# Optimization experiments

Measured on AMD Instinct MI355X. Metric: run time of the kernel, lower is better.

## Reference

```python
import jax, jax.numpy as jnp
import numpy as np

B, T, C, H = 16, 512, 256, 8
HS_T = C // H   # temporal head size = 32
HS_S = T // H   # spatial head size = 64
EPS = 1e-6


def _ln(x, w, b):
    m = x.mean(-1, keepdims=True)
    v = ((x - m) ** 2).mean(-1, keepdims=True)
    return (x - m) / jnp.sqrt(v + EPS) * w + b


def setup_inputs() -> dict:
    key = jax.random.key(0)
    ks = jax.random.split(key, 16)
    rn = lambda k, s, scale: jax.random.normal(k, s, dtype=jnp.float32) * scale
    inp = {
        "x_T": rn(ks[0], (B, T, C), 1.0),
        "x_S": rn(ks[1], (B, C, T), 1.0),
        # temporal attention: per-head q/k/v projections, stacked [H, hs, C]
        "Wq_t": rn(ks[2], (H, HS_T, C), C ** -0.5),
        "Wk_t": rn(ks[3], (H, HS_T, C), C ** -0.5),
        "Wv_t": rn(ks[4], (H, HS_T, C), C ** -0.5),
        "Wo": rn(ks[5], (C, C), C ** -0.5),
        # spatial attention: per-head q/k over the time axis, stacked [H, hs_s, T]
        "Wq_s": rn(ks[6], (H, HS_S, T), T ** -0.5),
        "Wk_s": rn(ks[7], (H, HS_S, T), T ** -0.5),
        # feed-forward blocks (expansion_factor=4)
        "ff1_w1": rn(ks[8], (4 * C, C), C ** -0.5),
        "ff1_b1": jnp.zeros((4 * C,), jnp.float32),
        "ff1_w2": rn(ks[9], (C, 4 * C), (4 * C) ** -0.5),
        "ff1_b2": jnp.zeros((C,), jnp.float32),
        "ff2_w1": rn(ks[10], (4 * C, C), C ** -0.5),
        "ff2_b1": jnp.zeros((4 * C,), jnp.float32),
        "ff2_w2": rn(ks[11], (C, 4 * C), (4 * C) ** -0.5),
        "ff2_b2": jnp.zeros((C,), jnp.float32),
        # layernorm affine params
        "t_ln1_w": jnp.ones((C,), jnp.float32), "t_ln1_b": jnp.zeros((C,), jnp.float32),
        "t_ln2_w": jnp.ones((C,), jnp.float32), "t_ln2_b": jnp.zeros((C,), jnp.float32),
        "s_ln1_w": jnp.ones((T,), jnp.float32), "s_ln1_b": jnp.zeros((T,), jnp.float32),
        "fus_ln_w": jnp.ones((C,), jnp.float32), "fus_ln_b": jnp.zeros((C,), jnp.float32),
    }
    return inp


def reference(x_T, x_S, Wq_t, Wk_t, Wv_t, Wo, Wq_s, Wk_s,
              ff1_w1, ff1_b1, ff1_w2, ff1_b2, ff2_w1, ff2_b1, ff2_w2, ff2_b2,
              t_ln1_w, t_ln1_b, t_ln2_w, t_ln2_b, s_ln1_w, s_ln1_b,
              fus_ln_w, fus_ln_b):
    # ---- temporal (causal) multi-head attention ----
    h = _ln(x_T, t_ln1_w, t_ln1_b)                         # [B,T,C]
    q = jnp.einsum('btc,hdc->bhtd', h, Wq_t)
    k = jnp.einsum('btc,hdc->bhtd', h, Wk_t)
    v = jnp.einsum('btc,hdc->bhtd', h, Wv_t)
    scores = jnp.einsum('bhtd,bhsd->bhts', q, k) / jnp.sqrt(jnp.float32(HS_T))
    causal = jnp.tril(jnp.ones((T, T), dtype=bool))
    scores = jnp.where(causal, scores, -jnp.inf)
    att = jax.nn.softmax(scores, axis=-1)
    o = jnp.einsum('bhts,bhsd->bhtd', att, v)              # [B,H,T,hs]
    o = o.transpose(0, 2, 1, 3).reshape(B, T, C)           # concat heads
    attn_out = o @ Wo.T
    x = x_T + attn_out
    # FFN 1
    h2 = _ln(x, t_ln2_w, t_ln2_b)
    f = jax.nn.relu(h2 @ ff1_w1.T + ff1_b1) @ ff1_w2.T + ff1_b2
    temporal_out = x + f                                   # [B,T,C]
    # ---- spatial (non-causal) attention over neurons ----
    hs = _ln(x_S, s_ln1_w, s_ln1_b)                        # [B,C,T]
    qs = jnp.einsum('bct,hdt->bhcd', hs, Wq_s)
    ks = jnp.einsum('bct,hdt->bhcd', hs, Wk_s)
    sc = jnp.einsum('bhcd,bhed->bhce', qs, ks) / jnp.sqrt(jnp.float32(HS_S))
    spatial_weights = jax.nn.softmax(sc, axis=-1).mean(axis=1)   # [B,C,C], mean over heads
    # ---- fusion ----
    fused = jnp.einsum('bce,bte->btc', spatial_weights, temporal_out)
    x2 = temporal_out + fused
    h3 = _ln(x2, fus_ln_w, fus_ln_b)
    f2 = jax.nn.relu(h3 @ ff2_w1.T + ff2_b1) @ ff2_w2.T + ff2_b2
    out = x2 + f2
    return out, spatial_weights
```

## Files before the change

kernel.cpp:

```cpp
#include <hip/hip_runtime.h>
#include <hip/hip_bf16.h>

typedef __hip_bfloat16 bf16;
typedef __attribute__((ext_vector_type(8))) short short8;
typedef __attribute__((ext_vector_type(4))) float f32x4;

#define F_BIAS 1
#define F_RELU 2
#define F_RES  4

__device__ __forceinline__ void st_out(float* p, float v){ *p = v; }
__device__ __forceinline__ void st_out(bf16* p, float v){ *p = __float2bfloat16(v); }
__device__ __forceinline__ short f2bs(float f){
  bf16 h = __float2bfloat16(f);
  return *reinterpret_cast<short*>(&h);
}

__device__ __forceinline__ void gl_lds16(const void* g, void* l){
  __builtin_amdgcn_global_load_lds(
      (const __attribute__((address_space(1))) void*)g,
      (__attribute__((address_space(3))) void*)l, 16, 0, 0);
}

__device__ __forceinline__ void lgkm_barrier(){
  asm volatile("s_waitcnt lgkmcnt(0)" ::: "memory");
  __builtin_amdgcn_s_barrier();
}

struct ProArgs {
  const float* wsrc[10];
  bf16* wdst[10];
  const float *xT, *xS, *tl1w, *tl1b, *sl1w, *sl1b;
  bf16 *hT, *hS;
};

template<int RL>
__device__ __forceinline__ void wave_ln(bf16* __restrict__ dst,
    const float* __restrict__ src, const float* __restrict__ w,
    const float* __restrict__ bvec, int row){
  int lane = threadIdx.x & 63;
  const float* s = src + (size_t)row*RL;
  float4 v0 = *(const float4*)(s + lane*4);
  float4 v1 = {0.f,0.f,0.f,0.f};
  float sum = v0.x+v0.y+v0.z+v0.w;
  float sq  = v0.x*v0.x+v0.y*v0.y+v0.z*v0.z+v0.w*v0.w;
  if (RL == 512){
    v1 = *(const float4*)(s + 256 + lane*4);
    sum += v1.x+v1.y+v1.z+v1.w;
    sq  += v1.x*v1.x+v1.y*v1.y+v1.z*v1.z+v1.w*v1.w;
  }
  #pragma unroll
  for (int off=32; off; off>>=1){
    sum += __shfl_xor(sum, off, 64);
    sq  += __shfl_xor(sq , off, 64);
  }
  const float inv = 1.0f/(float)RL;
  float mean = sum*inv;
  float rstd = rsqrtf(sq*inv - mean*mean + 1e-6f);
  float4 w0 = *(const float4*)(w + lane*4);
  float4 b0 = *(const float4*)(bvec + lane*4);
  bf16* d = dst + (size_t)row*RL;
  short4 o;
  o.x = f2bs((v0.x-mean)*rstd*w0.x + b0.x);
  o.y = f2bs((v0.y-mean)*rstd*w0.y + b0.y);
  o.z = f2bs((v0.z-mean)*rstd*w0.z + b0.z);
  o.w = f2bs((v0.w-mean)*rstd*w0.w + b0.w);
  *(short4*)((short*)d + lane*4) = o;
  if (RL == 512){
    float4 w1 = *(const float4*)(w + 256 + lane*4);
    float4 b1 = *(const float4*)(bvec + 256 + lane*4);
    short4 o1;
    o1.x = f2bs((v1.x-mean)*rstd*w1.x + b1.x);
    o1.y = f2bs((v1.y-mean)*rstd*w1.y + b1.y);
    o1.z = f2bs((v1.z-mean)*rstd*w1.z + b1.z);
    o1.w = f2bs((v1.w-mean)*rstd*w1.w + b1.w);
    *(short4*)((short*)d + 256 + lane*4) = o1;
  }
}

__global__ __launch_bounds__(256) void prologue(ProArgs a){
  int blk = blockIdx.x;
  int wid = threadIdx.x >> 6;
  if (blk < 1792){
    int v = blk*256 + threadIdx.x;
    int e = v*4;
    int seg = (e>=65536)+(e>=131072)+(e>=196608)+(e>=262144)+(e>=524288)
            + (e>=786432)+(e>=1048576)+(e>=1310720)+(e>=1572864);
    const int starts[10] = {0,65536,131072,196608,262144,524288,786432,
                            1048576,1310720,1572864};
    int off = e - starts[seg];
    float4 f = *(const float4*)(a.wsrc[seg] + off);
    short4 o;
    o.x = f2bs(f.x); o.y = f2bs(f.y); o.z = f2bs(f.z); o.w = f2bs(f.w);
    *(short4*)((short*)a.wdst[seg] + off) = o;
  } else if (blk < 1792 + 2048){
    wave_ln<256>(a.hT, a.xT, a.tl1w, a.tl1b, (blk-1792)*4 + wid);
  } else {
    wave_ln<512>(a.hS, a.xS, a.sl1w, a.sl1b, (blk-3840)*4 + wid);
  }
}

template<int BM, int BN, int BK>
__device__ __forceinline__ void gemm_body(
    short* __restrict__ AsB, short* __restrict__ BsB,
    const bf16* __restrict__ A, const bf16* __restrict__ B,
    float* __restrict__ outF, bf16* __restrict__ outB,
    const float* __restrict__ bias, const float* __restrict__ resid,
    int K, int lda, int ldb, int ldc, int flags, int m0, int n0){
  int tid = threadIdx.x;
  int w = tid>>6, lane = tid&63, quad = lane>>4, l16 = lane&15;
  constexpr int MF  = BM/32;
  constexpr int NF  = BN/32;
  constexpr int CPR = BK/8;
  constexpr int CA  = BM*CPR/256;
  constexpr int CB  = BN*CPR/256;
  int wm = (w>>1)*(BM/2), wn = (w&1)*(BN/2);
  f32x4 acc[MF][NF];
  #pragma unroll
  for (int r=0;r<MF;r++)
    #pragma unroll
    for (int j=0;j<NF;j++)
      acc[r][j] = (f32x4){0.f,0.f,0.f,0.f};

  auto stage = [&](int k0, int half){
    short* as = AsB + half*(BM*BK);
    short* bs = BsB + half*(BN*BK);
    #pragma unroll
    for (int c=0;c<CA;c++){
      int ch = tid + c*256;
      int row = ch / CPR, p = ch % CPR;
      gl_lds16(A + (size_t)(m0+row)*lda + k0 + ((p ^ (row&(CPR-1)))*8),
               &as[row*BK + p*8]);
    }
    #pragma unroll
    for (int c=0;c<CB;c++){
      int ch = tid + c*256;
      int row = ch / CPR, p = ch % CPR;
      gl_lds16(B + (size_t)(n0+row)*ldb + k0 + ((p ^ (row&(CPR-1)))*8),
               &bs[row*BK + p*8]);
    }
  };

  stage(0, 0);
  int nk = K / BK;
  for (int t = 0; t < nk; ++t){
    __syncthreads();
    if (t+1 < nk) stage((t+1)*BK, (t+1)&1);
    const short* as = AsB + (t&1)*(BM*BK);
    const short* bs = BsB + (t&1)*(BN*BK);
    #pragma unroll
    for (int ks=0; ks<BK/32; ++ks){
      short8 af[MF], bfr[NF];
      #pragma unroll
      for (int r=0;r<MF;r++){
        int rr = wm + r*16 + l16;
        af[r] = *(short8*)&as[rr*BK + (((ks*4+quad) ^ (rr&(CPR-1)))*8)];
      }
      #pragma unroll
      for (int j=0;j<NF;j++){
        int rr = wn + j*16 + l16;
        bfr[j] = *(short8*)&bs[rr*BK + (((ks*4+quad) ^ (rr&(CPR-1)))*8)];
      }
      #pragma unroll
      for (int r=0;r<MF;r++)
        #pragma unroll
        for (int j=0;j<NF;j++)
          acc[r][j] = __builtin_amdgcn_mfma_f32_16x16x32_bf16(af[r], bfr[j], acc[r][j], 0,0,0);
    }
  }
  #pragma unroll
  for (int r=0;r<MF;r++){
    int mb = m0 + wm + r*16 + quad*4;
    #pragma unroll
    for (int j=0;j<NF;j++){
      int n = n0 + wn + j*16 + l16;
      float bv = (flags & F_BIAS) ? bias[n] : 0.0f;
      #pragma unroll
      for (int e=0;e<4;e++){
        float v = acc[r][j][e] + bv;
        if (flags & F_RELU) v = fmaxf(v, 0.0f);
        long long idx = (long long)(mb+e)*ldc + n;
        if (flags & F_RES) v += resid[idx];
        if (outF) outF[idx] = v;
        if (outB) st_out(outB + idx, v);
      }
    }
  }
}

struct GArgs {
  const bf16 *A, *B;
  float* outF; bf16* outB;
  const float *bias, *resid;
  int K, lda, ldb, ldc, flags, ty;
};
__global__ __launch_bounds__(256) void gemm_dual(GArgs g0, GArgs g1, int n0){
  __shared__ __align__(16) short As[2*128*64];
  __shared__ __align__(16) short Bs[2*128*64];
  int id = blockIdx.x;
  bool first = id < n0;
  const GArgs& g = first ? g0 : g1;
  int t = first ? id : id - n0;
  int bx = t / g.ty, by = t - bx*g.ty;
  gemm_body<128,128,64>(As, Bs, g.A, g.B, g.outF, g.outB, g.bias, g.resid,
                        g.K, g.lda, g.ldb, g.ldc, g.flags, bx*128, by*128);
}

struct LnFfnArgs {
  const bf16 *A;
  const bf16 *Bm;
  const float *resid0;
  const float *lnw, *lnb;
  const bf16 *W1; const float *B1;
  const bf16 *W2; const float *B2;
  float *outF; bf16 *outB;
  long long sA, sB, sR, sO;
};

__global__ __launch_bounds__(512) void lnffn(LnFfnArgs a){
  __shared__ __align__(16) short arena[73728];
  __shared__ float redS[4][32], redQ[4][32];
  int bz = blockIdx.z;
  const bf16* A  = a.A  + (size_t)bz*a.sA;
  const bf16* Bm = a.Bm + (size_t)bz*a.sB;
  long long rbase = (long long)bz*a.sR;
  long long obase = (long long)bz*a.sO;
  int tid = threadIdx.x;
  int w = tid>>6, lane = tid&63, quad = lane>>4, l16 = lane&15;
  int m0 = blockIdx.x*32;
  int wm = (w>>2)*16;
  int wn = (w&3)*64;

  short* As  = arena;
  short* Bs  = arena + 4096;
  short* Hin = arena;
  short* Hs  = arena + 8192;
  short* Bst = arena + 40960;

  f32x4 acc[4];
  #pragma unroll
  for (int j=0;j<4;j++) acc[j] = (f32x4){0.f,0.f,0.f,0.f};

  auto stage0 = [&](int k0, int half){
    short* as = As + half*(32*64);
    short* bs = Bs + half*(256*64);
    if (tid < 256){
      int row = tid >> 3, p = tid & 7;
      gl_lds16(A + (size_t)(m0+row)*256 + k0 + ((p ^ (row&7))*8),
               &as[row*64 + p*8]);
    }
    #pragma unroll
    for (int c=0;c<4;c++){
      int ch = tid + c*512;
      int row = ch >> 3, p = ch & 7;
      gl_lds16(Bm + (size_t)row*256 + k0 + ((p ^ (row&7))*8),
               &bs[row*64 + p*8]);
    }
  };

  stage0(0, 0);
  for (int t = 0; t < 4; ++t){
    __syncthreads();
    if (t+1 < 4) stage0((t+1)*64, (t+1)&1);
    const short* as = As + (t&1)*(32*64);
    const short* bs = Bs + (t&1)*(256*64);
    #pragma unroll
    for (int ks=0; ks<2; ++ks){
      int rr = wm + l16;
      short8 af = *(short8*)&as[rr*64 + (((ks*4+quad) ^ (rr&7))*8)];
      #pragma unroll
      for (int j=0;j<4;j++){
        int rb = wn + j*16 + l16;
        short8 bfr = *(short8*)&bs[rb*64 + (((ks*4+quad) ^ (rb&7))*8)];
        acc[j] = __builtin_amdgcn_mfma_f32_16x16x32_bf16(af, bfr, acc[j], 0,0,0);
      }
    }
  }
  #pragma unroll
  for (int e=0;e<4;e++){
    int row = wm + quad*4 + e;
    float s = 0.f, q2 = 0.f;
    #pragma unroll
    for (int j=0;j<4;j++){
      float v = acc[j][e] + a.resid0[rbase + (long long)(m0+row)*256 + wn + j*16 + l16];
      acc[j][e] = v;
      s += v; q2 += v*v;
    }
    #pragma unroll
    for (int off=1; off<16; off<<=1){
      s  += __shfl_xor(s , off, 16);
      q2 += __shfl_xor(q2, off, 16);
    }
    if (l16==0){ redS[w&3][row] = s; redQ[w&3][row] = q2; }
  }
  __syncthreads();
  #pragma unroll
  for (int e=0;e<4;e++){
    int row = wm + quad*4 + e;
    float tot = redS[0][row] + redS[1][row] + redS[2][row] + redS[3][row];
    float tq  = redQ[0][row] + redQ[1][row] + redQ[2][row] + redQ[3][row];
    float mean = tot * (1.0f/256.0f);
    float var  = tq * (1.0f/256.0f) - mean*mean;
    float rstd = rsqrtf(var + 1e-6f);
    #pragma unroll
    for (int j=0;j<4;j++){
      int col = wn + j*16 + l16;
      float h = (acc[j][e]-mean)*rstd*a.lnw[col] + a.lnb[col];
      int g = col >> 3;
      Hin[row*256 + ((g ^ row)*8) + (col&7)] = f2bs(h);
    }
  }

  auto stageA = [&](int i, int half){
    short* bs = Bst + half*16384;
    int nc = i>>2, kt = i&3;
    #pragma unroll
    for (int c=0;c<2;c++){
      int ch = tid + c*512;
      int row = ch>>3, p = ch&7;
      gl_lds16(a.W1 + (size_t)(nc*128+row)*256 + kt*64 + ((p ^ (row&7))*8),
               &bs[ch*8]);
    }
  };
  stageA(0, 0);
  f32x4 a2[2];
  for (int i=0; i<32; ++i){
    __syncthreads();
    if (i+1 < 32) stageA(i+1, (i+1)&1);
    const short* bs = Bst + (i&1)*16384;
    int kt = i&3, nc = i>>2;
    if (kt==0){
      a2[0] = (f32x4){0.f,0.f,0.f,0.f};
      a2[1] = (f32x4){0.f,0.f,0.f,0.f};
    }
    #pragma unroll
    for (int ks=0; ks<2; ++ks){
      int rr = wm + l16;
      int kk = kt*8 + ks*4 + quad;
      short8 af = *(short8*)&Hin[rr*256 + ((kk ^ rr)*8)];
      #pragma unroll
      for (int j=0;j<2;j++){
        int rb = (w&3)*32 + j*16 + l16;
        short8 bk = *(short8*)&bs[rb*64 + (((ks*4+quad) ^ (rb&7))*8)];
        a2[j] = __builtin_amdgcn_mfma_f32_16x16x32_bf16(af, bk, a2[j], 0,0,0);
      }
    }
    if (kt==3){
      #pragma unroll
      for (int j=0;j<2;j++)
        #pragma unroll
        for (int e=0;e<4;e++){
          int row = wm + quad*4 + e;
          int col = nc*128 + (w&3)*32 + j*16 + l16;
          float v = fmaxf(a2[j][e] + a.B1[col], 0.0f);
          int g = col>>3;
          Hs[row*1024 + ((g ^ (row&7))*8) + (col&7)] = f2bs(v);
        }
    }
  }

  auto stageB = [&](int kt, int half){
    short* bs = Bst + half*16384;
    #pragma unroll
    for (int c=0;c<4;c++){
      int ch = tid + c*512;
      int row = ch>>3, p = ch&7;
      gl_lds16(a.W2 + (size_t)row*1024 + kt*64 + ((p ^ (row&7))*8),
               &bs[ch*8]);
    }
  };
  stageB(0, 0);
  f32x4 accB[4];
  #pragma unroll
  for (int j=0;j<4;j++) accB[j] = (f32x4){0.f,0.f,0.f,0.f};
  for (int kt=0; kt<16; ++kt){
    __syncthreads();
    if (kt+1 < 16) stageB(kt+1, (kt+1)&1);
    const short* bs = Bst + (kt&1)*16384;
    #pragma unroll
    for (int ks=0; ks<2; ++ks){
      int rr = wm + l16;
      int kk = kt*8 + ks*4 + quad;
      short8 af = *(short8*)&Hs[rr*1024 + ((kk ^ (rr&7))*8)];
      #pragma unroll
      for (int j=0;j<4;j++){
        int rb = wn + j*16 + l16;
        short8 bk = *(short8*)&bs[rb*64 + (((ks*4+quad) ^ (rb&7))*8)];
        accB[j] = __builtin_amdgcn_mfma_f32_16x16x32_bf16(af, bk, accB[j], 0,0,0);
      }
    }
  }
  #pragma unroll
  for (int j=0;j<4;j++){
    int n = wn + j*16 + l16;
    float bv = a.B2[n];
    #pragma unroll
    for (int e=0;e<4;e++){
      int row = wm + quad*4 + e;
      long long idx = obase + (long long)(m0+row)*256 + n;
      float v = accB[j][e] + bv + acc[j][e];
      a.outF[idx] = v;
      if (a.outB) st_out(a.outB + idx, v);
    }
  }
}

__device__ __forceinline__ int fsw(int row){ return (row>>1)&3; }
__global__ __launch_bounds__(256) void flash_mfma(
    const bf16* __restrict__ qkv, bf16* __restrict__ o){
  int qt = (int)gridDim.x - 1 - (int)blockIdx.x;
  int h = blockIdx.y, b = blockIdx.z;
  int tid = threadIdx.x;
  int w = tid>>6, lane = tid&63, quad = lane>>4, l16 = lane&15;
  __shared__ __align__(16) bf16 Qs[64*32];
  __shared__ __align__(16) bf16 Ks[2][64*32];
  __shared__ __align__(16) bf16 Vt[2][32*72];
  __shared__ __align__(16) bf16 Ps[64*72];
  const bf16* base = qkv + (size_t)b*512*768;
  int t0 = qt*64;
  int srow = tid>>2, spos = tid&3;
  gl_lds16(base + (size_t)(t0+srow)*768 + h*32 + ((spos ^ fsw(srow))*8),
           &Qs[srow*32 + spos*8]);
  {
    const bf16* rp = base + (size_t)srow*768 + h*32;
    gl_lds16(rp + 256 + ((spos ^ fsw(srow))*8), &Ks[0][srow*32 + spos*8]);
    short8 v = *(const short8*)(rp + 512 + spos*8);
    #pragma unroll
    for (int q=0;q<8;q++){
      short tmp = v[q];
      Vt[0][(spos*8+q)*72 + srow] = *(bf16*)&tmp;
    }
  }
  f32x4 accO[2];
  accO[0] = (f32x4){0.f,0.f,0.f,0.f};
  accO[1] = (f32x4){0.f,0.f,0.f,0.f};
  float m_i[4], l_i[4];
  #pragma unroll
  for (int e=0;e<4;e++){ m_i[e] = -3.0e38f; l_i[e] = 0.0f; }
  const float scale = 0.17677669529663687f;
  __syncthreads();
  int rq = w*16 + l16;
  short8 aq = *(short8*)&Qs[rq*32 + ((quad ^ fsw(rq))*8)];

  for (int kt = 0; kt <= qt; ++kt){
    if (kt) __syncthreads();
    int cur = kt&1, nxt = cur^1;
    bool pre = (kt < qt);
    short8 vpre;
    if (pre){
      const bf16* rp = base + (size_t)((kt+1)*64 + srow)*768 + h*32;
      gl_lds16(rp + 256 + ((spos ^ fsw(srow))*8), &Ks[nxt][srow*32 + spos*8]);
      vpre = *(const short8*)(rp + 512 + spos*8);
    }
    f32x4 S[4];
    #pragma unroll
    for (int j2=0;j2<4;j2++){
      int rk = j2*16 + l16;
      short8 bk = *(short8*)&Ks[cur][rk*32 + ((quad ^ fsw(rk))*8)];
      S[j2] = __builtin_amdgcn_mfma_f32_16x16x32_bf16(aq, bk,
                (f32x4){0.f,0.f,0.f,0.f}, 0,0,0);
    }
    bool diag = (kt == qt);
    int s0 = kt*64;
    int qrow_base = t0 + w*16 + quad*4;
    #pragma unroll
    for (int e=0;e<4;e++){
      float sv[4];
      #pragma unroll
      for (int j2=0;j2<4;j2++){
        float x = S[j2][e]*scale;
        if (diag && (s0 + j2*16 + l16 > qrow_base + e)) x = -3.0e38f;
        sv[j2] = x;
      }
      float mx = fmaxf(fmaxf(sv[0],sv[1]), fmaxf(sv[2],sv[3]));
      #pragma unroll
      for (int off=1; off<16; off<<=1) mx = fmaxf(mx, __shfl_xor(mx, off, 64));
      float m_new = fmaxf(m_i[e], mx);
      float alpha = __expf(m_i[e]-m_new);
      float rs = 0.0f;
      #pragma unroll
      for (int j2=0;j2<4;j2++){
        float p = __expf(sv[j2]-m_new);
        rs += p;
        Ps[(w*16+quad*4+e)*72 + j2*16 + l16] = __float2bfloat16(p);
      }
      #pragma unroll
      for (int off=1; off<16; off<<=1) rs += __shfl_xor(rs, off, 64);
      l_i[e] = l_i[e]*alpha + rs;
      m_i[e] = m_new;
      accO[0][e] *= alpha;
      accO[1][e] *= alpha;
    }
    asm volatile("s_waitcnt lgkmcnt(0)" ::: "memory");
    __builtin_amdgcn_sched_barrier(0);
    #pragma unroll
    for (int sh=0; sh<2; ++sh){
      short8 ap = *(short8*)&Ps[(w*16+l16)*72 + sh*32 + quad*8];
      #pragma unroll
      for (int dh=0; dh<2; ++dh){
        short8 bv = *(short8*)&Vt[cur][(dh*16+l16)*72 + sh*32 + quad*8];
        accO[dh] = __builtin_amdgcn_mfma_f32_16x16x32_bf16(ap, bv, accO[dh], 0,0,0);
      }
    }
    if (pre){
      #pragma unroll
      for (int q=0;q<8;q++){
        short tmp = vpre[q];
        Vt[nxt][(spos*8+q)*72 + srow] = *(bf16*)&tmp;
      }
    }
  }
  #pragma unroll
  for (int e=0;e<4;e++){
    float inv = 1.0f/l_i[e];
    int t = t0 + w*16 + quad*4 + e;
    bf16* op = o + ((size_t)(b*512+t))*256 + h*32 + l16;
    op[0]  = __float2bfloat16(accO[0][e]*inv);
    op[16] = __float2bfloat16(accO[1][e]*inv);
  }
}

__global__ __launch_bounds__(256) void spatial_fused(
    const bf16* __restrict__ qk, float* __restrict__ out1,
    bf16* __restrict__ swB){
  int ct = blockIdx.x & 15, b = blockIdx.x >> 4;
  int tid = threadIdx.x;
  int w = tid>>6, lane = tid&63, quad = lane>>4, l16 = lane&15;
  __shared__ __align__(16) bf16 Qall[16*512];
  __shared__ __align__(16) bf16 Ks[2][256*64];
  __shared__ float redM[4][16], redS2[4][16];
  const bf16* qbase = qk + ((size_t)(b*256 + ct*16))*1024;
  #pragma unroll
  for (int c=0;c<4;c++){
    int ch = tid + c*256;
    int row = ch>>6, p = ch&63;
    gl_lds16(qbase + (size_t)row*1024 + ((p ^ (row&7))*8), &Qall[row*512 + p*8]);
  }
  auto stageK = [&](int h, int half){
    bf16* ks = Ks[half];
    #pragma unroll
    for (int c=0;c<8;c++){
      int ch = tid + c*256;
      int e = ch>>3, p = ch&7;
      gl_lds16(qk + ((size_t)(b*256 + e))*1024 + 512 + h*64 + ((p ^ (e&7))*8),
               &ks[e*64 + p*8]);
    }
  };
  stageK(0, 0);
  float fRes[4][4];
  #pragma unroll
  for (int j=0;j<4;j++)
    #pragma unroll
    for (int e=0;e<4;e++) fRes[j][e] = 0.0f;

  for (int h=0; h<8; ++h){
    __syncthreads();
    if (h+1 < 8) stageK(h+1, (h+1)&1);
    const bf16* kcur = Ks[h&1];
    f32x4 acc[4];
    #pragma unroll
    for (int j=0;j<4;j++) acc[j] = (f32x4){0.f,0.f,0.f,0.f};
    #pragma unroll
    for (int ki=0; ki<2; ++ki){
      int g = h*8 + ki*4 + quad;
      short8 aq = *(short8*)&Qall[l16*512 + ((g ^ (l16&7))*8)];
      #pragma unroll
      for (int j=0;j<4;j++){
        int e = w*64 + j*16 + l16;
        short8 bk = *(short8*)&kcur[e*64 + (((ki*4+quad) ^ (e&7))*8)];
        acc[j] = __builtin_amdgcn_mfma_f32_16x16x32_bf16(aq, bk, acc[j], 0,0,0);
      }
    }
    #pragma unroll
    for (int e=0;e<4;e++){
      float m = -3.0e38f;
      #pragma unroll
      for (int j=0;j<4;j++){
        float s = acc[j][e]*0.125f;
        acc[j][e] = s;
        m = fmaxf(m, s);
      }
      #pragma unroll
      for (int off=1; off<16; off<<=1) m = fmaxf(m, __shfl_xor(m, off, 16));
      if (l16==0) redM[w][quad*4+e] = m;
    }
    lgkm_barrier();
    #pragma unroll
    for (int e=0;e<4;e++){
      int r = quad*4+e;
      float m = fmaxf(fmaxf(redM[0][r],redM[1][r]), fmaxf(redM[2][r],redM[3][r]));
      float s = 0.0f;
      #pragma unroll
      for (int j=0;j<4;j++){
        float p = __expf(acc[j][e]-m);
        acc[j][e] = p; s += p;
      }
      #pragma unroll
      for (int off=1; off<16; off<<=1) s += __shfl_xor(s, off, 16);
      if (l16==0) redS2[w][r] = s;
    }
    lgkm_barrier();
    #pragma unroll
    for (int e=0;e<4;e++){
      int r = quad*4+e;
      float tot = redS2[0][r]+redS2[1][r]+redS2[2][r]+redS2[3][r];
      float inv = 0.125f/tot;
      #pragma unroll
      for (int j=0;j<4;j++) fRes[j][e] += acc[j][e]*inv;
    }
  }
  #pragma unroll
  for (int e=0;e<4;e++){
    int c = ct*16 + quad*4 + e;
    size_t rb = ((size_t)b*256 + c)*256;
    #pragma unroll
    for (int j=0;j<4;j++){
      int col = w*64 + j*16 + l16;
      out1[rb+col] = fRes[j][e];
      swB[rb+col]  = __float2bfloat16(fRes[j][e]);
    }
  }
}

extern "C" void kernel_launch(void* const* d_in, const int* in_sizes, int n_in,
                              void* d_out, int out_size, void* d_ws, size_t ws_size,
                              hipStream_t stream){
  (void)in_sizes; (void)n_in; (void)out_size; (void)ws_size;
  const float* x_T  = (const float*)d_in[0];
  const float* x_S  = (const float*)d_in[1];
  const float* Wq_t = (const float*)d_in[2];
  const float* Wk_t = (const float*)d_in[3];
  const float* Wv_t = (const float*)d_in[4];
  const float* Wo   = (const float*)d_in[5];
  const float* Wq_s = (const float*)d_in[6];
  const float* Wk_s = (const float*)d_in[7];
  const float* f1w1 = (const float*)d_in[8];
  const float* f1b1 = (const float*)d_in[9];
  const float* f1w2 = (const float*)d_in[10];
  const float* f1b2 = (const float*)d_in[11];
  const float* f2w1 = (const float*)d_in[12];
  const float* f2b1 = (const float*)d_in[13];
  const float* f2w2 = (const float*)d_in[14];
  const float* f2b2 = (const float*)d_in[15];
  const float* tl1w = (const float*)d_in[16];
  const float* tl1b = (const float*)d_in[17];
  const float* tl2w = (const float*)d_in[18];
  const float* tl2b = (const float*)d_in[19];
  const float* sl1w = (const float*)d_in[20];
  const float* sl1b = (const float*)d_in[21];
  const float* flw  = (const float*)d_in[22];
  const float* flb  = (const float*)d_in[23];

  float* ws = (float*)d_ws;
  size_t off = 0;
  bf16*  Wqkvb  = (bf16*)(ws + off); off += 768*256/2;
  bf16*  Wob    = (bf16*)(ws + off); off += 256*256/2;
  bf16*  f1w1b  = (bf16*)(ws + off); off += 1024*256/2;
  bf16*  f1w2b  = (bf16*)(ws + off); off += 256*1024/2;
  bf16*  f2w1b  = (bf16*)(ws + off); off += 1024*256/2;
  bf16*  f2w2b  = (bf16*)(ws + off); off += 256*1024/2;
  bf16*  WSb    = (bf16*)(ws + off); off += 1024*512/2;
  bf16*  bufHb  = (bf16*)(ws + off); off += (size_t)8192*256/2;
  bf16*  bufHSb = (bf16*)(ws + off); off += (size_t)4096*512/2;
  bf16*  bufQKVb= (bf16*)(ws + off); off += (size_t)8192*768/2;
  bf16*  bufOb  = (bf16*)(ws + off); off += (size_t)8192*256/2;
  bf16*  bufTOb = (bf16*)(ws + off); off += (size_t)8192*256/2;
  bf16*  swB    = (bf16*)(ws + off); off += (size_t)16*256*256/2;
  bf16*  qkB    = (bf16*)(ws + off); off += (size_t)4096*1024/2;
  float* bufTO  = ws + off; off += (size_t)8192*256;

  float* out0 = (float*)d_out;
  float* out1 = out0 + (size_t)16*512*256;

  ProArgs pa;
  pa.wsrc[0]=Wq_t;  pa.wdst[0]=Wqkvb;
  pa.wsrc[1]=Wk_t;  pa.wdst[1]=Wqkvb+65536;
  pa.wsrc[2]=Wv_t;  pa.wdst[2]=Wqkvb+131072;
  pa.wsrc[3]=Wo;    pa.wdst[3]=Wob;
  pa.wsrc[4]=f1w1;  pa.wdst[4]=f1w1b;
  pa.wsrc[5]=f1w2;  pa.wdst[5]=f1w2b;
  pa.wsrc[6]=f2w1;  pa.wdst[6]=f2w1b;
  pa.wsrc[7]=f2w2;  pa.wdst[7]=f2w2b;
  pa.wsrc[8]=Wq_s;  pa.wdst[8]=WSb;
  pa.wsrc[9]=Wk_s;  pa.wdst[9]=WSb+262144;
  pa.xT=x_T; pa.xS=x_S; pa.tl1w=tl1w; pa.tl1b=tl1b;
  pa.sl1w=sl1w; pa.sl1b=sl1b; pa.hT=bufHb; pa.hS=bufHSb;
  prologue<<<4864,256,0,stream>>>(pa);

  GArgs gq, gs;
  gq.A=bufHb;  gq.B=Wqkvb; gq.outF=nullptr; gq.outB=bufQKVb;
  gq.bias=nullptr; gq.resid=nullptr;
  gq.K=256; gq.lda=256; gq.ldb=256; gq.ldc=768; gq.flags=0; gq.ty=6;
  gs.A=bufHSb; gs.B=WSb;   gs.outF=nullptr; gs.outB=qkB;
  gs.bias=nullptr; gs.resid=nullptr;
  gs.K=512; gs.lda=512; gs.ldb=512; gs.ldc=1024; gs.flags=0; gs.ty=8;
  gemm_dual<<<640,256,0,stream>>>(gq, gs, 384);

  spatial_fused<<<256,256,0,stream>>>(qkB, out1, swB);

  flash_mfma<<<dim3(8,8,16),256,0,stream>>>(bufQKVb, bufOb);

  LnFfnArgs la1;
  la1.A=bufOb; la1.Bm=Wob; la1.resid0=x_T; la1.lnw=tl2w; la1.lnb=tl2b;
  la1.W1=f1w1b; la1.B1=f1b1; la1.W2=f1w2b; la1.B2=f1b2;
  la1.outF=bufTO; la1.outB=bufTOb;
  la1.sA=0; la1.sB=0; la1.sR=0; la1.sO=0;
  lnffn<<<dim3(256,1,1),512,0,stream>>>(la1);

  LnFfnArgs la2;
  la2.A=bufTOb; la2.Bm=swB; la2.resid0=bufTO; la2.lnw=flw; la2.lnb=flb;
  la2.W1=f2w1b; la2.B1=f2b1; la2.W2=f2w2b; la2.B2=f2b2;
  la2.outF=out0; la2.outB=nullptr;
  la2.sA=131072; la2.sB=65536; la2.sR=131072; la2.sO=131072;
  lnffn<<<dim3(16,1,16),512,0,stream>>>(la2);
}
```

Before: 285.6 us.

## Load FFN weights directly from global into registers and retile lnffn warps

The fused residual+LayerNorm+FFN kernel stops staging the A/B operands and the W1/W2 weight tiles through double-buffered LDS with per-tile barriers. Instead each wave reads its MFMA fragments straight from global memory (relying on cache for reuse). Each of the 8 waves now covers all 32 rows and a 32-column slice, or a 128-column slice for the hidden layer. The LDS arena shrinks to just the LN output and hidden activations, with the reduction scratch aliased into the hidden buffer. This removes most __syncthreads and could allow more blocks per CU. The cost is exposed global-load latency without software pipelining and redundant weight fetches across blocks.

```diff
diff --git a/kernel.cpp b/kernel.cpp
--- a/kernel.cpp
+++ b/kernel.cpp
@@ -218,8 +218,10 @@
 };
 
 __global__ __launch_bounds__(512) void lnffn(LnFfnArgs a){
-  __shared__ __align__(16) short arena[73728];
-  __shared__ float redS[4][32], redQ[4][32];
+  __shared__ __align__(16) short Hin[32*256];
+  __shared__ __align__(16) short Hs[32*1024];
+  float (*redS)[32] = (float(*)[32])Hs;
+  float (*redQ)[32] = (float(*)[32])(Hs + 512);
   int bz = blockIdx.z;
   const bf16* A  = a.A  + (size_t)bz*a.sA;
   const bf16* Bm = a.Bm + (size_t)bz*a.sB;
@@ -228,181 +230,150 @@
   int tid = threadIdx.x;
   int w = tid>>6, lane = tid&63, quad = lane>>4, l16 = lane&15;
   int m0 = blockIdx.x*32;
-  int wm = (w>>2)*16;
-  int wn = (w&3)*64;
-
-  short* As  = arena;
-  short* Bs  = arena + 4096;
-  short* Hin = arena;
-  short* Hs  = arena + 8192;
-  short* Bst = arena + 40960;
-
-  f32x4 acc[4];
-  #pragma unroll
-  for (int j=0;j<4;j++) acc[j] = (f32x4){0.f,0.f,0.f,0.f};
-
-  auto stage0 = [&](int k0, int half){
-    short* as = As + half*(32*64);
-    short* bs = Bs + half*(256*64);
-    if (tid < 256){
-      int row = tid >> 3, p = tid & 7;
-      gl_lds16(A + (size_t)(m0+row)*256 + k0 + ((p ^ (row&7))*8),
-               &as[row*64 + p*8]);
-    }
-    #pragma unroll
-    for (int c=0;c<4;c++){
-      int ch = tid + c*512;
-      int row = ch >> 3, p = ch & 7;
-      gl_lds16(Bm + (size_t)row*256 + k0 + ((p ^ (row&7))*8),
-               &bs[row*64 + p*8]);
-    }
-  };
-
-  stage0(0, 0);
-  for (int t = 0; t < 4; ++t){
-    __syncthreads();
-    if (t+1 < 4) stage0((t+1)*64, (t+1)&1);
-    const short* as = As + (t&1)*(32*64);
-    const short* bs = Bs + (t&1)*(256*64);
-    #pragma unroll
-    for (int ks=0; ks<2; ++ks){
-      int rr = wm + l16;
-      short8 af = *(short8*)&as[rr*64 + (((ks*4+quad) ^ (rr&7))*8)];
+
+  f32x4 acc0[2][2];
+  #pragma unroll
+  for (int r=0;r<2;r++)
+    #pragma unroll
+    for (int j=0;j<2;j++) acc0[r][j] = (f32x4){0.f,0.f,0.f,0.f};
+  #pragma unroll
+  for (int ks=0; ks<8; ++ks){
+    short8 af[2], bk[2];
+    #pragma unroll
+    for (int r=0;r<2;r++)
+      af[r] = *(const short8*)(A + (size_t)(m0 + r*16 + l16)*256 + ks*32 + quad*8);
+    #pragma unroll
+    for (int j=0;j<2;j++)
+      bk[j] = *(const short8*)(Bm + (size_t)(w*32 + j*16 + l16)*256 + ks*32 + quad*8);
+    #pragma unroll
+    for (int r=0;r<2;r++)
+      #pragma unroll
+      for (int j=0;j<2;j++)
+        acc0[r][j] = __builtin_amdgcn_mfma_f32_16x16x32_bf16(af[r], bk[j], acc0[r][j], 0,0,0);
+  }
+  #pragma unroll
+  for (int r=0;r<2;r++)
+    #pragma unroll
+    for (int e=0;e<4;e++){
+      int row = r*16 + quad*4 + e;
+      float s = 0.f, q2 = 0.f;
+      #pragma unroll
+      for (int j=0;j<2;j++){
+        float v = acc0[r][j][e] +
+                  a.resid0[rbase + (long long)(m0+row)*256 + w*32 + j*16 + l16];
+        acc0[r][j][e] = v;
+        s += v; q2 += v*v;
+      }
+      #pragma unroll
+      for (int off=1; off<16; off<<=1){
+        s  += __shfl_xor(s , off, 16);
+        q2 += __shfl_xor(q2, off, 16);
+      }
+      if (l16==0){ redS[w][row] = s; redQ[w][row] = q2; }
+    }
+  __syncthreads();
+  #pragma unroll
+  for (int r=0;r<2;r++)
+    #pragma unroll
+    for (int e=0;e<4;e++){
+      int row = r*16 + quad*4 + e;
+      float tot = 0.f, tq = 0.f;
+      #pragma unroll
+      for (int ww=0; ww<8; ww++){ tot += redS[ww][row]; tq += redQ[ww][row]; }
+      float mean = tot * (1.0f/256.0f);
+      float var  = tq * (1.0f/256.0f) - mean*mean;
+      float rstd = rsqrtf(var + 1e-6f);
+      #pragma unroll
+      for (int j=0;j<2;j++){
+        int col = w*32 + j*16 + l16;
+        float h = (acc0[r][j][e]-mean)*rstd*a.lnw[col] + a.lnb[col];
+        int g = col >> 3;
+        Hin[row*256 + ((g ^ row)*8) + (col&7)] = f2bs(h);
+      }
+    }
+  __syncthreads();
+
+  for (int hc=0; hc<2; ++hc){
+    f32x4 acc1[2][4];
+    #pragma unroll
+    for (int r=0;r<2;r++)
+      #pragma unroll
+      for (int j=0;j<4;j++) acc1[r][j] = (f32x4){0.f,0.f,0.f,0.f};
+    #pragma unroll
+    for (int ks=0; ks<8; ++ks){
+      short8 af[2], bk[4];
+      #pragma unroll
+      for (int r=0;r<2;r++){
+        int rr = r*16 + l16;
+        int kk = ks*4 + quad;
+        af[r] = *(short8*)&Hin[rr*256 + ((kk ^ rr)*8)];
+      }
       #pragma unroll
       for (int j=0;j<4;j++){
-        int rb = wn + j*16 + l16;
-        short8 bfr = *(short8*)&bs[rb*64 + (((ks*4+quad) ^ (rb&7))*8)];
-        acc[j] = __builtin_amdgcn_mfma_f32_16x16x32_bf16(af, bfr, acc[j], 0,0,0);
-      }
-    }
-  }
-  #pragma unroll
-  for (int e=0;e<4;e++){
-    int row = wm + quad*4 + e;
-    float s = 0.f, q2 = 0.f;
-    #pragma unroll
-    for (int j=0;j<4;j++){
-      float v = acc[j][e] + a.resid0[rbase + (long long)(m0+row)*256 + wn + j*16 + l16];
-      acc[j][e] = v;
-      s += v; q2 += v*v;
-    }
-    #pragma unroll
-    for (int off=1; off<16; off<<=1){
-      s  += __shfl_xor(s , off, 16);
-      q2 += __shfl_xor(q2, off, 16);
-    }
-    if (l16==0){ redS[w&3][row] = s; redQ[w&3][row] = q2; }
-  }
-  __syncthreads();
-  #pragma unroll
-  for (int e=0;e<4;e++){
-    int row = wm + quad*4 + e;
-    float tot = redS[0][row] + redS[1][row] + redS[2][row] + redS[3][row];
-    float tq  = redQ[0][row] + redQ[1][row] + redQ[2][row] + redQ[3][row];
-    float mean = tot * (1.0f/256.0f);
-    float var  = tq * (1.0f/256.0f) - mean*mean;
-    float rstd = rsqrtf(var + 1e-6f);
-    #pragma unroll
-    for (int j=0;j<4;j++){
-      int col = wn + j*16 + l16;
-      float h = (acc[j][e]-mean)*rstd*a.lnw[col] + a.lnb[col];
-      int g = col >> 3;
-      Hin[row*256 + ((g ^ row)*8) + (col&7)] = f2bs(h);
-    }
-  }
-
-  auto stageA = [&](int i, int half){
-    short* bs = Bst + half*16384;
-    int nc = i>>2, kt = i&3;
-    #pragma unroll
-    for (int c=0;c<2;c++){
-      int ch = tid + c*512;
-      int row = ch>>3, p = ch&7;
-      gl_lds16(a.W1 + (size_t)(nc*128+row)*256 + kt*64 + ((p ^ (row&7))*8),
-               &bs[ch*8]);
-    }
-  };
-  stageA(0, 0);
-  f32x4 a2[2];
-  for (int i=0; i<32; ++i){
-    __syncthreads();
-    if (i+1 < 32) stageA(i+1, (i+1)&1);
-    const short* bs = Bst + (i&1)*16384;
-    int kt = i&3, nc = i>>2;
-    if (kt==0){
-      a2[0] = (f32x4){0.f,0.f,0.f,0.f};
-      a2[1] = (f32x4){0.f,0.f,0.f,0.f};
-    }
-    #pragma unroll
-    for (int ks=0; ks<2; ++ks){
-      int rr = wm + l16;
-      int kk = kt*8 + ks*4 + quad;
-      short8 af = *(short8*)&Hin[rr*256 + ((kk ^ rr)*8)];
-      #pragma unroll
-      for (int j=0;j<2;j++){
-        int rb = (w&3)*32 + j*16 + l16;
-        short8 bk = *(short8*)&bs[rb*64 + (((ks*4+quad) ^ (rb&7))*8)];
-        a2[j] = __builtin_amdgcn_mfma_f32_16x16x32_bf16(af, bk, a2[j], 0,0,0);
-      }
-    }
-    if (kt==3){
-      #pragma unroll
-      for (int j=0;j<2;j++)
+        int hr = w*128 + hc*64 + j*16 + l16;
+        bk[j] = *(const short8*)(a.W1 + (size_t)hr*256 + ks*32 + quad*8);
+      }
+      #pragma unroll
+      for (int r=0;r<2;r++)
+        #pragma unroll
+        for (int j=0;j<4;j++)
+          acc1[r][j] = __builtin_amdgcn_mfma_f32_16x16x32_bf16(af[r], bk[j], acc1[r][j], 0,0,0);
+    }
+    #pragma unroll
+    for (int r=0;r<2;r++)
+      #pragma unroll
+      for (int j=0;j<4;j++)
         #pragma unroll
         for (int e=0;e<4;e++){
-          int row = wm + quad*4 + e;
-          int col = nc*128 + (w&3)*32 + j*16 + l16;
-          float v = fmaxf(a2[j][e] + a.B1[col], 0.0f);
+          int row = r*16 + quad*4 + e;
+          int col = w*128 + hc*64 + j*16 + l16;
+          float v = fmaxf(acc1[r][j][e] + a.B1[col], 0.0f);
           int g = col>>3;
           Hs[row*1024 + ((g ^ (row&7))*8) + (col&7)] = f2bs(v);
         }
-    }
-  }
-
-  auto stageB = [&](int kt, int half){
-    short* bs = Bst + half*16384;
-    #pragma unroll
-    for (int c=0;c<4;c++){
-      int ch = tid + c*512;
-      int row = ch>>3, p = ch&7;
-      gl_lds16(a.W2 + (size_t)row*1024 + kt*64 + ((p ^ (row&7))*8),
-               &bs[ch*8]);
-    }
-  };
-  stageB(0, 0);
-  f32x4 accB[4];
-  #pragma unroll
-  for (int j=0;j<4;j++) accB[j] = (f32x4){0.f,0.f,0.f,0.f};
-  for (int kt=0; kt<16; ++kt){
-    __syncthreads();
-    if (kt+1 < 16) stageB(kt+1, (kt+1)&1);
-    const short* bs = Bst + (kt&1)*16384;
-    #pragma unroll
-    for (int ks=0; ks<2; ++ks){
-      int rr = wm + l16;
-      int kk = kt*8 + ks*4 + quad;
-      short8 af = *(short8*)&Hs[rr*1024 + ((kk ^ (rr&7))*8)];
-      #pragma unroll
-      for (int j=0;j<4;j++){
-        int rb = wn + j*16 + l16;
-        short8 bk = *(short8*)&bs[rb*64 + (((ks*4+quad) ^ (rb&7))*8)];
-        accB[j] = __builtin_amdgcn_mfma_f32_16x16x32_bf16(af, bk, accB[j], 0,0,0);
-      }
-    }
-  }
-  #pragma unroll
-  for (int j=0;j<4;j++){
-    int n = wn + j*16 + l16;
-    float bv = a.B2[n];
-    #pragma unroll
-    for (int e=0;e<4;e++){
-      int row = wm + quad*4 + e;
-      long long idx = obase + (long long)(m0+row)*256 + n;
-      float v = accB[j][e] + bv + acc[j][e];
-      a.outF[idx] = v;
-      if (a.outB) st_out(a.outB + idx, v);
-    }
-  }
+  }
+  __syncthreads();
+
+  f32x4 accB[2][2];
+  #pragma unroll
+  for (int r=0;r<2;r++)
+    #pragma unroll
+    for (int j=0;j<2;j++) accB[r][j] = (f32x4){0.f,0.f,0.f,0.f};
+  #pragma unroll 8
+  for (int ks=0; ks<32; ++ks){
+    short8 af[2], bk[2];
+    #pragma unroll
+    for (int r=0;r<2;r++){
+      int rr = r*16 + l16;
+      int kk = ks*4 + quad;
+      af[r] = *(short8*)&Hs[rr*1024 + ((kk ^ (rr&7))*8)];
+    }
+    #pragma unroll
+    for (int j=0;j<2;j++){
+      int n = w*32 + j*16 + l16;
+      bk[j] = *(const short8*)(a.W2 + (size_t)n*1024 + ks*32 + quad*8);
+    }
+    #pragma unroll
+    for (int r=0;r<2;r++)
+      #pragma unroll
+      for (int j=0;j<2;j++)
+        accB[r][j] = __builtin_amdgcn_mfma_f32_16x16x32_bf16(af[r], bk[j], accB[r][j], 0,0,0);
+  }
+  #pragma unroll
+  for (int r=0;r<2;r++)
+    #pragma unroll
+    for (int j=0;j<2;j++){
+      int n = w*32 + j*16 + l16;
+      float bv = a.B2[n];
+      #pragma unroll
+      for (int e=0;e<4;e++){
+        int row = r*16 + quad*4 + e;
+        long long idx = obase + (long long)(m0+row)*256 + n;
+        float v = accB[r][j][e] + bv + acc0[r][j][e];
+        a.outF[idx] = v;
+        if (a.outB) st_out(a.outB + idx, v);
+      }
+    }
 }
 
 __device__ __forceinline__ int fsw(int row){ return (row>>1)&3; }
```

Result: no change. 284.9 us (-0.3%).
